# Performance work log

Measured on AMD Instinct MI355X. Metric: run time of the kernel, lower is better.

## Reference

```python
import jax, jax.numpy as jnp
import numpy as np

HIDDEN = 768
E_ROUTED = 32
K_ACT = 4
E_SHARED = 8
RANK = 64
FFN_ROUTED = HIDDEN * 2
FFN_SHARED = HIDDEN * 3


def setup_inputs() -> dict:
    key = jax.random.key(0)
    ks = jax.random.split(key, 8)
    s = 0.02
    return {
        "x": jax.random.normal(ks[0], (2, 2048, HIDDEN), dtype=jnp.float32),
        # shared experts: SwiGLU (gate, up, down), stacked over experts
        "shared_wg": jax.random.normal(ks[1], (E_SHARED, HIDDEN, FFN_SHARED), dtype=jnp.float32) * s,
        "shared_wu": jax.random.normal(ks[2], (E_SHARED, HIDDEN, FFN_SHARED), dtype=jnp.float32) * s,
        "shared_wd": jax.random.normal(ks[3], (E_SHARED, FFN_SHARED, HIDDEN), dtype=jnp.float32) * s,
        # routed experts: Linear -> GELU -> Linear, stacked
        "routed_w1": jax.random.normal(ks[4], (E_ROUTED, HIDDEN, FFN_ROUTED), dtype=jnp.float32) * s,
        "routed_w2": jax.random.normal(ks[5], (E_ROUTED, FFN_ROUTED, HIDDEN), dtype=jnp.float32) * s,
        # low-rank router
        "router_down": jax.random.normal(ks[6], (HIDDEN, RANK), dtype=jnp.float32) * s,
        "router_up": jax.random.normal(ks[7], (RANK, E_ROUTED), dtype=jnp.float32) * s,
    }


def reference(x, shared_wg, shared_wu, shared_wd, routed_w1, routed_w2, router_down, router_up):
    B, S, D = x.shape
    xf = x.reshape(-1, D)  # [T, D]

    # shared experts (SwiGLU), averaged
    g = jnp.einsum('td,edh->eth', xf, shared_wg)
    u = jnp.einsum('td,edh->eth', xf, shared_wu)
    sh = jnp.einsum('eth,ehd->etd', jax.nn.silu(g) * u, shared_wd)
    shared_output = sh.mean(axis=0)  # [T, D] (sum / num_shared_expert)

    # low-rank router + top-k
    router_logits = (xf @ router_down) @ router_up  # [T, E]
    routing_weights, selected = jax.lax.top_k(router_logits, K_ACT)  # [T, K]
    routing_weights = jax.nn.softmax(routing_weights, axis=-1)

    # dense all-expert FFN (faithful to source), then gather top-k (== one-hot einsum)
    h = jnp.einsum('td,edh->eth', xf, routed_w1)
    expert_outputs = jnp.einsum('eth,ehd->etd', jax.nn.gelu(h, approximate=False), routed_w2)  # [E,T,D]
    sel_out = jnp.take_along_axis(expert_outputs.transpose(1, 0, 2), selected[:, :, None], axis=1)  # [T,K,D]
    routed_output = jnp.einsum('tkd,tk->td', sel_out, routing_weights)

    output = (shared_output + routed_output).reshape(B, S, D)

    # aux losses
    counts = jnp.bincount(selected.reshape(-1), length=E_ROUTED).astype(jnp.float32)
    load_balance_loss = jnp.var(counts, ddof=1)  # torch .var() is unbiased
    probs = jax.nn.softmax(router_logits, axis=-1)
    router_entropy = -(probs * jnp.log(probs + 1e-10)).sum(-1).mean()
    shared_norm = jnp.linalg.norm(shared_output, axis=-1).mean()
    routed_norm = jnp.linalg.norm(routed_output, axis=-1).mean()
    balance_loss = jnp.abs(shared_norm - routed_norm)

    return output, load_balance_loss, router_entropy, balance_loss
```

## Files before the change

### kernel.cpp

```cpp
#include <hip/hip_runtime.h>
#include <hip/hip_bf16.h>
#include <math.h>


#define T_TOK 4096
#define DHID 768
#define NE_R 32
#define NE_S 8
#define F_S 2304
#define F_R 1536
#define MAXROWS 20480
#define MAX_TILES 160

typedef float f32x4 __attribute__((ext_vector_type(4)));
typedef short s16x8 __attribute__((ext_vector_type(8)));

__device__ __forceinline__ short f2bf(float f) {
  union { float f; unsigned u; } v; v.f = f;
  unsigned r = v.u + 0x7fffu + ((v.u >> 16) & 1u);
  return (short)(r >> 16);
}

#define GLD16(gsrc, ldst)                                                     \
  __builtin_amdgcn_global_load_lds(                                           \
      (const __attribute__((address_space(1))) void*)(gsrc),                  \
      (__attribute__((address_space(3))) void*)(ldst), 16, 0, 0)

__global__ __launch_bounds__(256) void cvt_x_kernel(const float* __restrict__ in,
    short* __restrict__ out, int* __restrict__ tlist, float* __restrict__ wslot,
    int* __restrict__ counts, int* __restrict__ cursor) {
  int i = blockIdx.x * 256 + threadIdx.x;
  if (i < T_TOK * DHID / 4) {
    float4 v = ((const float4*)in)[i];
    short4 o;
    o.x = f2bf(v.x); o.y = f2bf(v.y); o.z = f2bf(v.z); o.w = f2bf(v.w);
    ((short4*)out)[i] = o;
  }
  if (i < MAXROWS) { tlist[i] = 0; wslot[i] = 0.f; }
  if (i < 32) { counts[i] = 0; cursor[i] = 0; }
}

__global__ __launch_bounds__(256) void transpose_shared(
    const float* __restrict__ swg, const float* __restrict__ swu,
    const float* __restrict__ swd, short* __restrict__ wgT,
    short* __restrict__ wuT, short* __restrict__ wdT) {
  int bid = blockIdx.x;
  const float* in; short* out; int R, C, nbx; long ldo;
  if (bid < 13824)      { in = swg; out = wgT; R = DHID; C = F_S; ldo = DHID; nbx = 72; }
  else if (bid < 27648) { bid -= 13824; in = swu; out = wuT; R = DHID; C = F_S; ldo = DHID; nbx = 72; }
  else                  { bid -= 27648; in = swd; out = wdT; R = F_S; C = DHID; ldo = F_S; nbx = 24; }
  int per = nbx * (R / 32);
  int b = bid / per, rem = bid % per;
  int c0 = (rem % nbx) * 32, r0 = (rem / nbx) * 32;
  in  += (size_t)b * R * C;
  out += (size_t)b * R * C;
  int tx = threadIdx.x & 31, ty = threadIdx.x >> 5;
  __shared__ float tile[32][33];
#pragma unroll
  for (int i = 0; i < 32; i += 8)
    tile[ty + i][tx] = in[(size_t)(r0 + ty + i) * C + (c0 + tx)];
  __syncthreads();
#pragma unroll
  for (int i = 0; i < 32; i += 8)
    out[(size_t)(c0 + ty + i) * ldo + (r0 + tx)] = f2bf(tile[tx][ty + i]);
}

__global__ __launch_bounds__(256) void transpose_routed(
    const float* __restrict__ rw1, const float* __restrict__ rw2,
    short* __restrict__ w1T, short* __restrict__ w2T) {
  int bid = blockIdx.x;
  const float* in; short* out; int R, C, nbx; long ldo;
  if (bid < 36864) { in = rw1; out = w1T; R = DHID; C = F_R; ldo = DHID; nbx = 48; }
  else             { bid -= 36864; in = rw2; out = w2T; R = F_R; C = DHID; ldo = F_R; nbx = 24; }
  int per = nbx * (R / 32);
  int b = bid / per, rem = bid % per;
  int c0 = (rem % nbx) * 32, r0 = (rem / nbx) * 32;
  in  += (size_t)b * R * C;
  out += (size_t)b * R * C;
  int tx = threadIdx.x & 31, ty = threadIdx.x >> 5;
  __shared__ float tile[32][33];
#pragma unroll
  for (int i = 0; i < 32; i += 8)
    tile[ty + i][tx] = in[(size_t)(r0 + ty + i) * C + (c0 + tx)];
  __syncthreads();
#pragma unroll
  for (int i = 0; i < 32; i += 8)
    out[(size_t)(c0 + ty + i) * ldo + (r0 + tx)] = f2bf(tile[tx][ty + i]);
}

__global__ __launch_bounds__(64) void router_kernel(const float* __restrict__ x,
    const float* __restrict__ rdown, const float* __restrict__ rup,
    int* __restrict__ sel, float* __restrict__ w4, int* __restrict__ counts,
    float* __restrict__ pent) {
  int t = blockIdx.x;
  int lane = threadIdx.x;
  __shared__ float xs[DHID];
  __shared__ float xrs[64];
  __shared__ float lg[32];
  const float* xt = x + (size_t)t * DHID;
  for (int i = lane; i < DHID; i += 64) xs[i] = xt[i];
  __syncthreads();
  float acc = 0.f;
#pragma unroll 8
  for (int d = 0; d < DHID; ++d) acc += xs[d] * rdown[d * 64 + lane];
  xrs[lane] = acc;
  __syncthreads();
  if (lane < 32) {
    float l = 0.f;
#pragma unroll 8
    for (int r = 0; r < 64; ++r) l += xrs[r] * rup[r * 32 + lane];
    lg[lane] = l;
  }
  __syncthreads();
  if (lane == 0) {
    int si[4]; float sv[4];
    unsigned taken = 0;
    for (int k = 0; k < 4; ++k) {
      float best = -3.4e38f; int bi = 0;
      for (int e = 0; e < 32; ++e)
        if (!((taken >> e) & 1u) && lg[e] > best) { best = lg[e]; bi = e; }
      taken |= 1u << bi; si[k] = bi; sv[k] = best;
    }
    float m = sv[0];
    float wv[4]; float zs = 0.f;
    for (int k = 0; k < 4; ++k) { wv[k] = __expf(sv[k] - m); zs += wv[k]; }
    for (int k = 0; k < 4; ++k) {
      sel[t * 4 + k] = si[k];
      w4[t * 4 + k] = wv[k] / zs;
      atomicAdd(&counts[si[k]], 1);
    }
    float Z = 0.f;
    for (int e = 0; e < 32; ++e) Z += __expf(lg[e] - m);
    float ent = 0.f;
    for (int e = 0; e < 32; ++e) {
      float p = __expf(lg[e] - m) / Z;
      ent -= p * logf(p + 1e-10f);
    }
    pent[t] = ent;
  }
}

__global__ void meta_kernel(const int* __restrict__ counts, int* __restrict__ meta) {
  if (threadIdx.x == 0) {
    int acc = 0;
    for (int e = 0; e < 32; ++e) { meta[e] = acc; acc += (counts[e] + 127) >> 7; }
    meta[32] = acc;
  }
}

__global__ __launch_bounds__(256) void build_kernel(const int* __restrict__ sel,
    const float* __restrict__ w4, const int* __restrict__ meta, int* __restrict__ cursor,
    int* __restrict__ tlist, float* __restrict__ wslot, int* __restrict__ pos) {
  int t = blockIdx.x * 256 + threadIdx.x;
  if (t >= T_TOK) return;
#pragma unroll
  for (int k = 0; k < 4; ++k) {
    int e = sel[t * 4 + k];
    int slot = atomicAdd(&cursor[e], 1);
    int g = meta[e] * 128 + slot;
    tlist[g] = t; wslot[g] = w4[t * 4 + k]; pos[t * 4 + k] = g;
  }
}

template<int MODE>
__global__ __launch_bounds__(256, MODE == 0 ? 2 : 3) void gemm_k(
    const short* __restrict__ A, const short* __restrict__ B, const short* __restrict__ B2,
    short* __restrict__ outH, float* __restrict__ outF, const float* __restrict__ wslot,
    const int* __restrict__ meta, const int* __restrict__ tlist,
    int K, int lda, long zbstride, long ldo, long ocolz, long orowz, long acolz) {
  constexpr int BM = 128, BN = 128;
  constexpr int WM = 64, WN = 64, FM = 4, FN = 4;
  __shared__ short As[BM * 64];
  __shared__ short Bs[BN * 64];
  __shared__ short Bs2[(MODE == 0) ? BN * 64 : 64];

  int tid = threadIdx.x;
  int wv = tid >> 6, lane = tid & 63;
  int wr = wv >> 1, wc = wv & 1;
  int lrow = lane & 15, kg = lane >> 4;
  int lrow7 = lrow & 7;
  int z = blockIdx.z;

  int bx = blockIdx.x, by = blockIdx.y;
  if constexpr (MODE == 0 || MODE == 2) {
    int gx = gridDim.x, gy = gridDim.y;
    int nwg = gx * gy;
    int orig = by * gx + bx;
    int swz = (orig & 7) * (nwg >> 3) + (orig >> 3);
    bx = swz / gy; by = swz % gy;
  }
  int n0 = bx * BN;

  int eidx = z;
  int g0 = 0, m0 = by * BM;
  if constexpr (MODE == 1 || MODE == 3) {
    int total = meta[32];
    int ty = blockIdx.y;
    if (ty >= total) return;
    int e = 0;
    while (meta[e + 1] <= ty) ++e;
    eidx = e;
    g0 = ty * BM;
  }

  int srow = tid >> 3;
  int scol = ((tid & 7) ^ (srow & 7)) * 8;

  f32x4 acc[FM][FN] = {};
  f32x4 acc2[(MODE == 0) ? FM : 1][(MODE == 0) ? FN : 1] = {};

  constexpr int EPB = (MODE == 2) ? 2 : 1;
#pragma unroll 1
  for (int ei = 0; ei < EPB; ++ei) {
    int e = (MODE == 2) ? (z * 2 + ei) : eidx;
    const short* Bb = B + (size_t)e * zbstride + (size_t)n0 * K;
    const short* B2b = (MODE == 0) ? (B2 + (size_t)e * zbstride + (size_t)n0 * K) : B;

    const short *as0, *as1, *as2, *as3;
    {
      auto arow = [&](int row) -> const short* {
        if constexpr (MODE == 1) {
          return A + (size_t)tlist[g0 + row] * lda + scol;
        } else if constexpr (MODE == 2) {
          return A + ((size_t)(m0 + row)) * lda + (size_t)e * acolz + scol;
        } else if constexpr (MODE == 3) {
          return A + ((size_t)(g0 + row)) * lda + scol;
        } else {
          return A + ((size_t)(m0 + row)) * lda + scol;
        }
      };
      as0 = arow(srow); as1 = arow(32 + srow); as2 = arow(64 + srow); as3 = arow(96 + srow);
    }
    const short* bs0 = Bb + (size_t)srow * K + scol;
    const short* bs1 = bs0 + (size_t)32 * K;
    const short* bs2 = bs0 + (size_t)64 * K;
    const short* bs3 = bs0 + (size_t)96 * K;
    const short* c2s0 = B2b + (size_t)srow * K + scol;
    const short* c2s1 = c2s0 + (size_t)32 * K;
    const short* c2s2 = c2s0 + (size_t)64 * K;
    const short* c2s3 = c2s0 + (size_t)96 * K;

    for (int kt = 0; kt < K; kt += 64) {
      GLD16(as0 + kt, As + (0 * 32 + wv * 8) * 64);
      GLD16(as1 + kt, As + (1 * 32 + wv * 8) * 64);
      GLD16(as2 + kt, As + (2 * 32 + wv * 8) * 64);
      GLD16(as3 + kt, As + (3 * 32 + wv * 8) * 64);
      GLD16(bs0 + kt, Bs + (0 * 32 + wv * 8) * 64);
      GLD16(bs1 + kt, Bs + (1 * 32 + wv * 8) * 64);
      GLD16(bs2 + kt, Bs + (2 * 32 + wv * 8) * 64);
      GLD16(bs3 + kt, Bs + (3 * 32 + wv * 8) * 64);
      if constexpr (MODE == 0) {
        GLD16(c2s0 + kt, Bs2 + (0 * 32 + wv * 8) * 64);
        GLD16(c2s1 + kt, Bs2 + (1 * 32 + wv * 8) * 64);
        GLD16(c2s2 + kt, Bs2 + (2 * 32 + wv * 8) * 64);
        GLD16(c2s3 + kt, Bs2 + (3 * 32 + wv * 8) * 64);
      }
      __syncthreads();
#pragma unroll
      for (int ks = 0; ks < 2; ++ks) {
        int pc = ((ks * 4 + kg) ^ lrow7) * 8;
        s16x8 af[FM], bb[FN];
#pragma unroll
        for (int i = 0; i < FM; ++i)
          af[i] = *(const s16x8*)&As[(wr * WM + i * 16 + lrow) * 64 + pc];
#pragma unroll
        for (int j = 0; j < FN; ++j)
          bb[j] = *(const s16x8*)&Bs[(wc * WN + j * 16 + lrow) * 64 + pc];
#pragma unroll
        for (int i = 0; i < FM; ++i)
#pragma unroll
          for (int j = 0; j < FN; ++j)
            acc[i][j] = __builtin_amdgcn_mfma_f32_16x16x32_bf16(af[i], bb[j], acc[i][j], 0, 0, 0);
        if constexpr (MODE == 0) {
          s16x8 b2[FN];
#pragma unroll
          for (int j = 0; j < FN; ++j)
            b2[j] = *(const s16x8*)&Bs2[(wc * WN + j * 16 + lrow) * 64 + pc];
#pragma unroll
          for (int i = 0; i < FM; ++i)
#pragma unroll
            for (int j = 0; j < FN; ++j)
              acc2[i][j] = __builtin_amdgcn_mfma_f32_16x16x32_bf16(af[i], b2[j], acc2[i][j], 0, 0, 0);
        }
      }
      __syncthreads();
    }
  }

#pragma unroll
  for (int i = 0; i < FM; ++i) {
#pragma unroll
    for (int r = 0; r < 4; ++r) {
      int rl = wr * WM + i * 16 + kg * 4 + r;
      float wsc = 0.f;
      if constexpr (MODE == 1) wsc = wslot[g0 + rl];
#pragma unroll
      for (int j = 0; j < FN; ++j) {
        int col = n0 + wc * WN + j * 16 + lrow;
        float v = acc[i][j][r];
        if constexpr (MODE == 0) {
          float u = acc2[i][j][r];
          float h = v / (1.f + __expf(-v)) * u;
          outH[(size_t)(m0 + rl) * ldo + (size_t)z * ocolz + col] = f2bf(h);
        } else if constexpr (MODE == 1) {
          float h = 0.5f * v * (1.f + erff(v * 0.70710678118f)) * wsc;
          outH[(size_t)(g0 + rl) * ldo + col] = f2bf(h);
        } else if constexpr (MODE == 2) {
          outF[(size_t)z * orowz + (size_t)(m0 + rl) * DHID + col] = v;
        } else {
          outF[(size_t)(g0 + rl) * DHID + col] = v;
        }
      }
    }
  }
}

__global__ __launch_bounds__(256) void combine_kernel(const float* __restrict__ spart,
    const float* __restrict__ Y, const int* __restrict__ pos,
    float* __restrict__ out, float* __restrict__ pnorm) {
  int t = blockIdx.x, tid = threadIdx.x;
  int p0 = pos[t * 4], p1 = pos[t * 4 + 1], p2 = pos[t * 4 + 2], p3 = pos[t * 4 + 3];
  size_t base = (size_t)t * DHID;
  float s2 = 0.f, r2 = 0.f;
  for (int d = tid; d < DHID; d += 256) {
    float s = 0.f;
#pragma unroll
    for (int e = 0; e < 4; ++e) s += spart[(size_t)e * T_TOK * DHID + base + d];
    s *= 0.125f;
    float r = Y[(size_t)p0 * DHID + d] + Y[(size_t)p1 * DHID + d] +
              Y[(size_t)p2 * DHID + d] + Y[(size_t)p3 * DHID + d];
    out[base + d] = s + r;
    s2 += s * s; r2 += r * r;
  }
  for (int o = 32; o > 0; o >>= 1) { s2 += __shfl_down(s2, o); r2 += __shfl_down(r2, o); }
  __shared__ float red[8];
  int wv = tid >> 6, lane = tid & 63;
  if (lane == 0) { red[wv] = s2; red[4 + wv] = r2; }
  __syncthreads();
  if (tid == 0) {
    float st = red[0] + red[1] + red[2] + red[3];
    float rt = red[4] + red[5] + red[6] + red[7];
    pnorm[t] = sqrtf(st);
    pnorm[T_TOK + t] = sqrtf(rt);
  }
}

__global__ __launch_bounds__(256) void finalize_kernel(const int* __restrict__ counts,
    const float* __restrict__ pent, const float* __restrict__ pnorm, float* __restrict__ o) {
  int tid = threadIdx.x;
  float es = 0.f, ss = 0.f, rs = 0.f;
  for (int i = tid; i < T_TOK; i += 256) {
    es += pent[i]; ss += pnorm[i]; rs += pnorm[T_TOK + i];
  }
  float vs = 0.f;
  if (tid < 32) { float d = (float)counts[tid] - 512.f; vs = d * d; }
  for (int off = 32; off > 0; off >>= 1) {
    es += __shfl_down(es, off); ss += __shfl_down(ss, off);
    rs += __shfl_down(rs, off); vs += __shfl_down(vs, off);
  }
  __shared__ float red[16];
  int wv = tid >> 6, lane = tid & 63;
  if (lane == 0) { red[wv] = es; red[4 + wv] = ss; red[8 + wv] = rs; red[12 + wv] = vs; }
  __syncthreads();
  if (tid == 0) {
    es = red[0] + red[1] + red[2] + red[3];
    ss = red[4] + red[5] + red[6] + red[7];
    rs = red[8] + red[9] + red[10] + red[11];
    vs = red[12] + red[13] + red[14] + red[15];
    o[0] = vs / 31.f;
    o[1] = es / (float)T_TOK;
    o[2] = fabsf(ss - rs) / (float)T_TOK;
  }
}

extern "C" void kernel_launch(void* const* d_in, const int* in_sizes, int n_in,
                              void* d_out, int out_size, void* d_ws, size_t ws_size,
                              hipStream_t stream) {
  const float* x   = (const float*)d_in[0];
  const float* swg = (const float*)d_in[1];
  const float* swu = (const float*)d_in[2];
  const float* swd = (const float*)d_in[3];
  const float* rw1 = (const float*)d_in[4];
  const float* rw2 = (const float*)d_in[5];
  const float* rdn = (const float*)d_in[6];
  const float* rup = (const float*)d_in[7];
  float* fout = (float*)d_out;

  char* w = (char*)d_ws;
  size_t off = 0;
  auto take = [&](size_t bytes) { char* p = w + off; off = (off + bytes + 255) & ~(size_t)255; return p; };
  short* xbf   = (short*)take((size_t)T_TOK * DHID * 2);
  int*   sel   = (int*)  take((size_t)T_TOK * 4 * 4);
  float* w4    = (float*)take((size_t)T_TOK * 4 * 4);
  int*   pos   = (int*)  take((size_t)T_TOK * 4 * 4);
  int*   counts= (int*)  take(32 * 4);
  int*   cursor= (int*)  take(32 * 4);
  int*   meta  = (int*)  take(64 * 4);
  int*   tlist = (int*)  take((size_t)MAXROWS * 4);
  float* wslot = (float*)take((size_t)MAXROWS * 4);
  float* pent  = (float*)take((size_t)T_TOK * 4);
  float* pnorm = (float*)take((size_t)2 * T_TOK * 4);
  float* spart = (float*)take((size_t)4 * T_TOK * DHID * 4);
  char*  arena = w + off;

  short* wgT = (short*)arena;
  short* wuT = wgT + (size_t)NE_S * F_S * DHID;
  short* wdT = wuT + (size_t)NE_S * F_S * DHID;
  short* Hsh = wdT + (size_t)NE_S * F_S * DHID;
  float* Y   = (float*)arena;
  short* w1T = (short*)(arena + (size_t)MAXROWS * DHID * 4);
  short* w2T = w1T + (size_t)NE_R * F_R * DHID;
  short* Hr  = w2T + (size_t)NE_R * F_R * DHID;

  cvt_x_kernel<<<(T_TOK * DHID / 4 + 255) / 256, 256, 0, stream>>>(x, xbf, tlist, wslot, counts, cursor);
  router_kernel<<<T_TOK, 64, 0, stream>>>(x, rdn, rup, sel, w4, counts, pent);
  meta_kernel<<<1, 64, 0, stream>>>(counts, meta);
  build_kernel<<<T_TOK / 256, 256, 0, stream>>>(sel, w4, meta, cursor, tlist, wslot, pos);

  transpose_shared<<<41472, 256, 0, stream>>>(swg, swu, swd, wgT, wuT, wdT);
  gemm_k<0><<<dim3(F_S / 128, T_TOK / 128, NE_S), 256, 0, stream>>>(
      xbf, wgT, wuT, Hsh, nullptr, nullptr, nullptr, nullptr,
      DHID, DHID, (long)F_S * DHID, (long)NE_S * F_S, (long)F_S, 0, 0);
  gemm_k<2><<<dim3(DHID / 128, T_TOK / 128, NE_S / 2), 256, 0, stream>>>(
      Hsh, wdT, nullptr, nullptr, spart, nullptr, nullptr, nullptr,
      F_S, NE_S * F_S, (long)DHID * F_S, DHID, 0, (long)T_TOK * DHID, (long)F_S);

  transpose_routed<<<73728, 256, 0, stream>>>(rw1, rw2, w1T, w2T);
  gemm_k<1><<<dim3(F_R / 128, MAX_TILES, 1), 256, 0, stream>>>(
      xbf, w1T, nullptr, Hr, nullptr, wslot, meta, tlist,
      DHID, DHID, (long)F_R * DHID, (long)F_R, 0, 0, 0);
  gemm_k<3><<<dim3(DHID / 128, MAX_TILES, 1), 256, 0, stream>>>(
      Hr, w2T, nullptr, nullptr, Y, nullptr, meta, tlist,
      F_R, F_R, (long)DHID * F_R, DHID, 0, 0, 0);

  combine_kernel<<<T_TOK, 256, 0, stream>>>(spart, Y, pos, fout, pnorm);
  finalize_kernel<<<1, 256, 0, stream>>>(counts, pent, pnorm, fout + (size_t)T_TOK * DHID);
}
```

Before: 906.6 us.

## Use 64x64 vectorized transpose tiles and narrow gate/up GEMM tile for occupancy

The weight transpose kernels now use 64x64 tiles and write four packed bf16 values per thread, which cuts block count and makes stores wider. The SwiGLU gate/up GEMM now handles 64 output columns per block, with gate and up halves sharing one B buffer and one accumulator array. This drops the second LDS buffer and accumulator set so all GEMM modes can run with launch bounds of 4 blocks per SU. The narrower tile means each A tile is reused by fewer output columns and twice as many blocks are launched. Forcing 4 blocks per unit may also cause register spills in the larger modes.

```diff
diff --git a/kernel.cpp b/kernel.cpp
--- a/kernel.cpp
+++ b/kernel.cpp
@@ -40,29 +40,39 @@
   if (i < 32) { counts[i] = 0; cursor[i] = 0; }
 }
 
+__device__ __forceinline__ void tile_transpose(const float* in, short* out,
+                                               int R, int C, long ldo,
+                                               int r0, int c0) {
+  __shared__ float tile[64][65];
+  int tx = threadIdx.x & 63, ty = threadIdx.x >> 6;
+#pragma unroll
+  for (int i = 0; i < 64; i += 4)
+    tile[ty + i][tx] = in[(size_t)(r0 + ty + i) * C + (c0 + tx)];
+  __syncthreads();
+  int u = threadIdx.x & 15, v = threadIdx.x >> 4;
+#pragma unroll
+  for (int i = 0; i < 64; i += 16) {
+    int c = v + i;
+    short4 o;
+    o.x = f2bf(tile[4 * u + 0][c]); o.y = f2bf(tile[4 * u + 1][c]);
+    o.z = f2bf(tile[4 * u + 2][c]); o.w = f2bf(tile[4 * u + 3][c]);
+    *(short4*)&out[(size_t)(c0 + c) * ldo + (r0 + 4 * u)] = o;
+  }
+}
+
 __global__ __launch_bounds__(256) void transpose_shared(
     const float* __restrict__ swg, const float* __restrict__ swu,
     const float* __restrict__ swd, short* __restrict__ wgT,
     short* __restrict__ wuT, short* __restrict__ wdT) {
   int bid = blockIdx.x;
   const float* in; short* out; int R, C, nbx; long ldo;
-  if (bid < 13824)      { in = swg; out = wgT; R = DHID; C = F_S; ldo = DHID; nbx = 72; }
-  else if (bid < 27648) { bid -= 13824; in = swu; out = wuT; R = DHID; C = F_S; ldo = DHID; nbx = 72; }
-  else                  { bid -= 27648; in = swd; out = wdT; R = F_S; C = DHID; ldo = F_S; nbx = 24; }
-  int per = nbx * (R / 32);
+  if (bid < 3456)      { in = swg; out = wgT; R = DHID; C = F_S; ldo = DHID; nbx = 36; }
+  else if (bid < 6912) { bid -= 3456; in = swu; out = wuT; R = DHID; C = F_S; ldo = DHID; nbx = 36; }
+  else                 { bid -= 6912; in = swd; out = wdT; R = F_S; C = DHID; ldo = F_S; nbx = 12; }
+  int per = nbx * (R / 64);
   int b = bid / per, rem = bid % per;
-  int c0 = (rem % nbx) * 32, r0 = (rem / nbx) * 32;
-  in  += (size_t)b * R * C;
-  out += (size_t)b * R * C;
-  int tx = threadIdx.x & 31, ty = threadIdx.x >> 5;
-  __shared__ float tile[32][33];
-#pragma unroll
-  for (int i = 0; i < 32; i += 8)
-    tile[ty + i][tx] = in[(size_t)(r0 + ty + i) * C + (c0 + tx)];
-  __syncthreads();
-#pragma unroll
-  for (int i = 0; i < 32; i += 8)
-    out[(size_t)(c0 + ty + i) * ldo + (r0 + tx)] = f2bf(tile[tx][ty + i]);
+  int c0 = (rem % nbx) * 64, r0 = (rem / nbx) * 64;
+  tile_transpose(in + (size_t)b * R * C, out + (size_t)b * R * C, R, C, ldo, r0, c0);
 }
 
 __global__ __launch_bounds__(256) void transpose_routed(
@@ -70,22 +80,12 @@
     short* __restrict__ w1T, short* __restrict__ w2T) {
   int bid = blockIdx.x;
   const float* in; short* out; int R, C, nbx; long ldo;
-  if (bid < 36864) { in = rw1; out = w1T; R = DHID; C = F_R; ldo = DHID; nbx = 48; }
-  else             { bid -= 36864; in = rw2; out = w2T; R = F_R; C = DHID; ldo = F_R; nbx = 24; }
-  int per = nbx * (R / 32);
+  if (bid < 9216) { in = rw1; out = w1T; R = DHID; C = F_R; ldo = DHID; nbx = 24; }
+  else            { bid -= 9216; in = rw2; out = w2T; R = F_R; C = DHID; ldo = F_R; nbx = 12; }
+  int per = nbx * (R / 64);
   int b = bid / per, rem = bid % per;
-  int c0 = (rem % nbx) * 32, r0 = (rem / nbx) * 32;
-  in  += (size_t)b * R * C;
-  out += (size_t)b * R * C;
-  int tx = threadIdx.x & 31, ty = threadIdx.x >> 5;
-  __shared__ float tile[32][33];
-#pragma unroll
-  for (int i = 0; i < 32; i += 8)
-    tile[ty + i][tx] = in[(size_t)(r0 + ty + i) * C + (c0 + tx)];
-  __syncthreads();
-#pragma unroll
-  for (int i = 0; i < 32; i += 8)
-    out[(size_t)(c0 + ty + i) * ldo + (r0 + tx)] = f2bf(tile[tx][ty + i]);
+  int c0 = (rem % nbx) * 64, r0 = (rem / nbx) * 64;
+  tile_transpose(in + (size_t)b * R * C, out + (size_t)b * R * C, R, C, ldo, r0, c0);
 }
 
 __global__ __launch_bounds__(64) void router_kernel(const float* __restrict__ x,
@@ -163,16 +163,15 @@
 }
 
 template<int MODE>
-__global__ __launch_bounds__(256, MODE == 0 ? 2 : 3) void gemm_k(
+__global__ __launch_bounds__(256, 4) void gemm_k(
     const short* __restrict__ A, const short* __restrict__ B, const short* __restrict__ B2,
     short* __restrict__ outH, float* __restrict__ outF, const float* __restrict__ wslot,
     const int* __restrict__ meta, const int* __restrict__ tlist,
     int K, int lda, long zbstride, long ldo, long ocolz, long orowz, long acolz) {
-  constexpr int BM = 128, BN = 128;
-  constexpr int WM = 64, WN = 64, FM = 4, FN = 4;
+  constexpr int BM = 128;
+  constexpr int WM = 64, FM = 4, FN = 4;
   __shared__ short As[BM * 64];
-  __shared__ short Bs[BN * 64];
-  __shared__ short Bs2[(MODE == 0) ? BN * 64 : 64];
+  __shared__ short Bs[128 * 64];
 
   int tid = threadIdx.x;
   int wv = tid >> 6, lane = tid & 63;
@@ -189,7 +188,7 @@
     int swz = (orig & 7) * (nwg >> 3) + (orig >> 3);
     bx = swz / gy; by = swz % gy;
   }
-  int n0 = bx * BN;
+  int n0 = bx * ((MODE == 0) ? 64 : 128);
 
   int eidx = z;
   int g0 = 0, m0 = by * BM;
@@ -207,14 +206,12 @@
   int scol = ((tid & 7) ^ (srow & 7)) * 8;
 
   f32x4 acc[FM][FN] = {};
-  f32x4 acc2[(MODE == 0) ? FM : 1][(MODE == 0) ? FN : 1] = {};
 
   constexpr int EPB = (MODE == 2) ? 2 : 1;
 #pragma unroll 1
   for (int ei = 0; ei < EPB; ++ei) {
     int e = (MODE == 2) ? (z * 2 + ei) : eidx;
     const short* Bb = B + (size_t)e * zbstride + (size_t)n0 * K;
-    const short* B2b = (MODE == 0) ? (B2 + (size_t)e * zbstride + (size_t)n0 * K) : B;
 
     const short *as0, *as1, *as2, *as3;
     {
@@ -233,12 +230,16 @@
     }
     const short* bs0 = Bb + (size_t)srow * K + scol;
     const short* bs1 = bs0 + (size_t)32 * K;
-    const short* bs2 = bs0 + (size_t)64 * K;
-    const short* bs3 = bs0 + (size_t)96 * K;
-    const short* c2s0 = B2b + (size_t)srow * K + scol;
-    const short* c2s1 = c2s0 + (size_t)32 * K;
-    const short* c2s2 = c2s0 + (size_t)64 * K;
-    const short* c2s3 = c2s0 + (size_t)96 * K;
+    const short* bs2;
+    const short* bs3;
+    if constexpr (MODE == 0) {
+      const short* B2b = B2 + (size_t)e * zbstride + (size_t)n0 * K;
+      bs2 = B2b + (size_t)srow * K + scol;
+      bs3 = bs2 + (size_t)32 * K;
+    } else {
+      bs2 = bs0 + (size_t)64 * K;
+      bs3 = bs0 + (size_t)96 * K;
+    }
 
     for (int kt = 0; kt < K; kt += 64) {
       GLD16(as0 + kt, As + (0 * 32 + wv * 8) * 64);
@@ -249,12 +250,6 @@
       GLD16(bs1 + kt, Bs + (1 * 32 + wv * 8) * 64);
       GLD16(bs2 + kt, Bs + (2 * 32 + wv * 8) * 64);
       GLD16(bs3 + kt, Bs + (3 * 32 + wv * 8) * 64);
-      if constexpr (MODE == 0) {
-        GLD16(c2s0 + kt, Bs2 + (0 * 32 + wv * 8) * 64);
-        GLD16(c2s1 + kt, Bs2 + (1 * 32 + wv * 8) * 64);
-        GLD16(c2s2 + kt, Bs2 + (2 * 32 + wv * 8) * 64);
-        GLD16(c2s3 + kt, Bs2 + (3 * 32 + wv * 8) * 64);
-      }
       __syncthreads();
 #pragma unroll
       for (int ks = 0; ks < 2; ++ks) {
@@ -264,24 +259,19 @@
         for (int i = 0; i < FM; ++i)
           af[i] = *(const s16x8*)&As[(wr * WM + i * 16 + lrow) * 64 + pc];
 #pragma unroll
-        for (int j = 0; j < FN; ++j)
-          bb[j] = *(const s16x8*)&Bs[(wc * WN + j * 16 + lrow) * 64 + pc];
+        for (int j = 0; j < FN; ++j) {
+          int brow;
+          if constexpr (MODE == 0)
+            brow = (j >= 2 ? 64 : 0) + wc * 32 + (j & 1) * 16 + lrow;
+          else
+            brow = wc * 64 + j * 16 + lrow;
+          bb[j] = *(const s16x8*)&Bs[brow * 64 + pc];
+        }
 #pragma unroll
         for (int i = 0; i < FM; ++i)
 #pragma unroll
           for (int j = 0; j < FN; ++j)
             acc[i][j] = __builtin_amdgcn_mfma_f32_16x16x32_bf16(af[i], bb[j], acc[i][j], 0, 0, 0);
-        if constexpr (MODE == 0) {
-          s16x8 b2[FN];
-#pragma unroll
-          for (int j = 0; j < FN; ++j)
-            b2[j] = *(const s16x8*)&Bs2[(wc * WN + j * 16 + lrow) * 64 + pc];
-#pragma unroll
-          for (int i = 0; i < FM; ++i)
-#pragma unroll
-            for (int j = 0; j < FN; ++j)
-              acc2[i][j] = __builtin_amdgcn_mfma_f32_16x16x32_bf16(af[i], b2[j], acc2[i][j], 0, 0, 0);
-        }
       }
       __syncthreads();
     }
@@ -294,21 +284,28 @@
       int rl = wr * WM + i * 16 + kg * 4 + r;
       float wsc = 0.f;
       if constexpr (MODE == 1) wsc = wslot[g0 + rl];
-#pragma unroll
-      for (int j = 0; j < FN; ++j) {
-        int col = n0 + wc * WN + j * 16 + lrow;
-        float v = acc[i][j][r];
-        if constexpr (MODE == 0) {
-          float u = acc2[i][j][r];
-          float h = v / (1.f + __expf(-v)) * u;
+      if constexpr (MODE == 0) {
+#pragma unroll
+        for (int jp = 0; jp < 2; ++jp) {
+          int col = n0 + wc * 32 + jp * 16 + lrow;
+          float g = acc[i][jp][r];
+          float u = acc[i][jp + 2][r];
+          float h = g / (1.f + __expf(-g)) * u;
           outH[(size_t)(m0 + rl) * ldo + (size_t)z * ocolz + col] = f2bf(h);
-        } else if constexpr (MODE == 1) {
-          float h = 0.5f * v * (1.f + erff(v * 0.70710678118f)) * wsc;
-          outH[(size_t)(g0 + rl) * ldo + col] = f2bf(h);
-        } else if constexpr (MODE == 2) {
-          outF[(size_t)z * orowz + (size_t)(m0 + rl) * DHID + col] = v;
-        } else {
-          outF[(size_t)(g0 + rl) * DHID + col] = v;
+        }
+      } else {
+#pragma unroll
+        for (int j = 0; j < FN; ++j) {
+          int col = n0 + wc * 64 + j * 16 + lrow;
+          float v = acc[i][j][r];
+          if constexpr (MODE == 1) {
+            float h = 0.5f * v * (1.f + erff(v * 0.70710678118f)) * wsc;
+            outH[(size_t)(g0 + rl) * ldo + col] = f2bf(h);
+          } else if constexpr (MODE == 2) {
+            outF[(size_t)z * orowz + (size_t)(m0 + rl) * DHID + col] = v;
+          } else if constexpr (MODE == 3) {
+            outF[(size_t)(g0 + rl) * DHID + col] = v;
+          }
         }
       }
     }
@@ -417,15 +414,15 @@
   meta_kernel<<<1, 64, 0, stream>>>(counts, meta);
   build_kernel<<<T_TOK / 256, 256, 0, stream>>>(sel, w4, meta, cursor, tlist, wslot, pos);
 
-  transpose_shared<<<41472, 256, 0, stream>>>(swg, swu, swd, wgT, wuT, wdT);
-  gemm_k<0><<<dim3(F_S / 128, T_TOK / 128, NE_S), 256, 0, stream>>>(
+  transpose_shared<<<10368, 256, 0, stream>>>(swg, swu, swd, wgT, wuT, wdT);
+  gemm_k<0><<<dim3(F_S / 64, T_TOK / 128, NE_S), 256, 0, stream>>>(
       xbf, wgT, wuT, Hsh, nullptr, nullptr, nullptr, nullptr,
       DHID, DHID, (long)F_S * DHID, (long)NE_S * F_S, (long)F_S, 0, 0);
   gemm_k<2><<<dim3(DHID / 128, T_TOK / 128, NE_S / 2), 256, 0, stream>>>(
       Hsh, wdT, nullptr, nullptr, spart, nullptr, nullptr, nullptr,
       F_S, NE_S * F_S, (long)DHID * F_S, DHID, 0, (long)T_TOK * DHID, (long)F_S);
 
-  transpose_routed<<<73728, 256, 0, stream>>>(rw1, rw2, w1T, w2T);
+  transpose_routed<<<18432, 256, 0, stream>>>(rw1, rw2, w1T, w2T);
   gemm_k<1><<<dim3(F_R / 128, MAX_TILES, 1), 256, 0, stream>>>(
       xbf, w1T, nullptr, Hr, nullptr, wslot, meta, tlist,
       DHID, DHID, (long)F_R * DHID, (long)F_R, 0, 0, 0);
```

New measurement: 910.3 us. Within noise of the previous version (+0.4%).
